# Optimization experiments

Hardware: AMD Instinct MI355X
Metric: run time of the kernel (lower is better)

Reference implementation:

```python
import jax, jax.numpy as jnp
import numpy as np
from jax import lax

N_INPUT, N_HIDDEN, N_OUTPUT = 1024, 2048, 1024
T, B = 512, 64

def setup_inputs() -> dict:
    key = jax.random.key(0)
    k_x, k_ih, k_hh, k_out = jax.random.split(key, 4)
    stdv = 1.0 / np.sqrt(N_HIDDEN)
    xs = jax.random.normal(k_x, (T, B, N_INPUT), dtype=jnp.float32)
    # torch nn.Linear weights are [out_features, in_features], init U(-stdv, stdv)
    W_ih = jax.random.uniform(k_ih, (N_HIDDEN, N_INPUT), jnp.float32, -stdv, stdv)
    W_hh = jax.random.uniform(k_hh, (N_HIDDEN, N_HIDDEN), jnp.float32, -stdv, stdv)
    W_out = jax.random.uniform(k_out, (N_OUTPUT, N_HIDDEN), jnp.float32, -stdv, stdv)
    return {"xs": xs, "W_ih": W_ih, "W_hh": W_hh, "W_out": W_out}

def reference(xs, W_ih, W_hh, W_out):
    # xs: [T, B, n_input] time-major. state starts as None -> relu(W_ih x),
    # which equals relu(W_ih x + W_hh * 0), so h0 = zeros is exact.
    n_hidden = W_hh.shape[0]
    h0 = jnp.zeros((xs.shape[1], n_hidden), dtype=xs.dtype)

    def step(h, x):
        h = jax.nn.relu(x @ W_ih.T + h @ W_hh.T)  # [B, n_hidden]
        return h, h

    _, h_seq = lax.scan(step, h0, xs)        # [T, B, n_hidden]
    ys = h_seq @ W_out.T                     # [T, B, n_output]
    return jnp.transpose(ys, (1, 0, 2))      # [B, T, n_output] (transpose(0,1))
```

## Files before the change

kernel.cpp:

```cpp
#include <hip/hip_runtime.h>
#include <hip/hip_bf16.h>
#include <stdint.h>


#define TT 512
#define BB 64
#define NIN 1024
#define NH 2048
#define NOUT 1024

typedef __attribute__((ext_vector_type(8))) short bf8;
typedef __attribute__((ext_vector_type(4))) float f4;
typedef __attribute__((ext_vector_type(4))) unsigned int u4;
typedef __attribute__((ext_vector_type(2))) unsigned long long ull2;

static __device__ __forceinline__ unsigned short f2bf(float f) {
  __hip_bfloat16 h = __float2bfloat16(f);
  return __builtin_bit_cast(unsigned short, h);
}
static __device__ __forceinline__ float bf2f(unsigned short v) {
  return __bfloat162float(__builtin_bit_cast(__hip_bfloat16, v));
}
static __device__ __forceinline__ u4 pack8(const float* f) {
  u4 r;
#pragma unroll
  for (int i = 0; i < 4; ++i) {
    unsigned lo = f2bf(f[2 * i]);
    unsigned hi = f2bf(f[2 * i + 1]);
    r[i] = lo | (hi << 16);
  }
  return r;
}

static __device__ __forceinline__ size_t sl_idx(int m, int col) {
  return (((size_t)(m >> 6) * 128 + (col >> 4)) << 10) + (size_t)(m & 63) * 16 + (col & 15);
}

template <bool ABF, bool TRANS>
__global__ void gemm_bt(const void* __restrict__ Av, const float* __restrict__ Bw,
                        void* __restrict__ Cv, int M, int N, int K) {
  constexpr int BM = 128, BN = 128, BK = 32;
  __shared__ u4 As[BM * 4];
  __shared__ u4 Bs[BN * 4];
  const int nt = N / BN;
  const int mi = (int)blockIdx.x / nt;
  const int ni = (int)blockIdx.x % nt;
  const int m0 = mi * BM, n0 = ni * BN;
  const int t = threadIdx.x;
  const int l = t & 63, w = t >> 6, wr = w >> 1, wc = w & 1;
  const int lr = l & 15, lq = l >> 4;

  f4 acc[4][4] = {};

  const int srow = t >> 1;
  const int sc0 = (t & 1) * 2;

  for (int kt = 0; kt < K; kt += BK) {
    if (ABF) {
      const unsigned short* A = (const unsigned short*)Av;
#pragma unroll
      for (int cc = 0; cc < 2; ++cc) {
        int c = sc0 + cc;
        u4 v = *(const u4*)(A + sl_idx(m0 + srow, kt + c * 8));
        As[srow * 4 + (c ^ ((srow ^ (srow >> 2)) & 3))] = v;
      }
    } else {
      const float* A = (const float*)Av;
#pragma unroll
      for (int cc = 0; cc < 2; ++cc) {
        int c = sc0 + cc;
        const float* p = A + (size_t)(m0 + srow) * K + kt + c * 8;
        float4 v0 = *(const float4*)p;
        float4 v1 = *(const float4*)(p + 4);
        float f[8] = {v0.x, v0.y, v0.z, v0.w, v1.x, v1.y, v1.z, v1.w};
        As[srow * 4 + (c ^ ((srow ^ (srow >> 2)) & 3))] = pack8(f);
      }
    }
#pragma unroll
    for (int cc = 0; cc < 2; ++cc) {
      int c = sc0 + cc;
      const float* p = Bw + (size_t)(n0 + srow) * K + kt + c * 8;
      float4 v0 = *(const float4*)p;
      float4 v1 = *(const float4*)(p + 4);
      float f[8] = {v0.x, v0.y, v0.z, v0.w, v1.x, v1.y, v1.z, v1.w};
      Bs[srow * 4 + (c ^ ((srow ^ (srow >> 2)) & 3))] = pack8(f);
    }
    __syncthreads();

    bf8 a[4], b[4];
#pragma unroll
    for (int i = 0; i < 4; ++i) {
      int ra = wr * 64 + i * 16 + lr;
      a[i] = __builtin_bit_cast(bf8, As[ra * 4 + (lq ^ ((ra ^ (ra >> 2)) & 3))]);
      int rb = wc * 64 + i * 16 + lr;
      b[i] = __builtin_bit_cast(bf8, Bs[rb * 4 + (lq ^ ((rb ^ (rb >> 2)) & 3))]);
    }
#pragma unroll
    for (int i = 0; i < 4; ++i)
#pragma unroll
      for (int j = 0; j < 4; ++j)
        acc[i][j] = __builtin_amdgcn_mfma_f32_16x16x32_bf16(a[i], b[j], acc[i][j], 0, 0, 0);
    __syncthreads();
  }

  if (TRANS) {
    float* C = (float*)Cv;
#pragma unroll
    for (int i = 0; i < 4; ++i)
#pragma unroll
      for (int j = 0; j < 4; ++j)
#pragma unroll
        for (int r = 0; r < 4; ++r) {
          int m = m0 + wr * 64 + i * 16 + lq * 4 + r;
          int n = n0 + wc * 64 + j * 16 + lr;
          C[(size_t)(m & 63) * (TT * NOUT) + (size_t)(m >> 6) * NOUT + n] = acc[i][j][r];
        }
  } else {
    unsigned short* C = (unsigned short*)Cv;
#pragma unroll
    for (int i = 0; i < 4; ++i)
#pragma unroll
      for (int j = 0; j < 4; ++j)
#pragma unroll
        for (int r = 0; r < 4; ++r) {
          int m = m0 + wr * 64 + i * 16 + lq * 4 + r;
          int n = n0 + wc * 64 + j * 16 + lr;
          C[sl_idx(m, n)] = f2bf(acc[i][j][r]);
        }
  }
}

__global__ __launch_bounds__(1024, 4) void rnn_recur(unsigned short* __restrict__ hseq,
                                                     const float* __restrict__ Whh,
                                                     unsigned* __restrict__ flags) {
  __shared__ u4 Wl[16 * 256];
  __shared__ float red[2][8][32][20];
  const int t = threadIdx.x;
  const int jb = (int)blockIdx.x & 127;
  const int bh = (int)blockIdx.x >> 7;
  const int j0 = jb * 16;

  {
    const int jl = t >> 6;
    const int c0 = (t & 63) * 4;
#pragma unroll
    for (int c = 0; c < 4; ++c) {
      int cc = c0 + c;
      const float* p = Whh + (size_t)(j0 + jl) * NH + cc * 8;
      float4 v0 = *(const float4*)p;
      float4 v1 = *(const float4*)(p + 4);
      float f[8] = {v0.x, v0.y, v0.z, v0.w, v1.x, v1.y, v1.z, v1.w};
      Wl[jl * 256 + (cc ^ (jl & 7))] = pack8(f);
    }
  }

  const int l = t & 63, w = t >> 6;
  const int lr = l & 15, lq = l >> 4;
  const int bg = w & 1, kg = w >> 1;
  const int row = bh * 32 + bg * 16 + lr;

  const int wrowL = bg * 16 + (l >> 2);
  const int wjq = l & 3;
  const size_t woff = (size_t)(bh * 32 + wrowL) * 16 + wjq * 4;

  unsigned long long pre = 0;

  __syncthreads();

  if (w < 2) {
    size_t e0 = ((size_t)jb << 10) + woff;
    unsigned long long p0 = *(const unsigned long long*)(hseq + e0);
    unsigned long long hv = 0;
#pragma unroll
    for (int i = 0; i < 4; ++i) {
      unsigned long long x = (p0 >> (16 * i)) & 0xffffull;
      if (!(x & 0x8000ull)) hv |= x << (16 * i);
    }
    __hip_atomic_store((unsigned long long*)(hseq + e0), hv, __ATOMIC_RELAXED,
                       __HIP_MEMORY_SCOPE_AGENT);
    asm volatile("s_waitcnt vmcnt(0)" ::: "memory");
    if (l == 0)
      __hip_atomic_store(flags + ((int)blockIdx.x * 2 + w), 1u, __ATOMIC_RELAXED,
                         __HIP_MEMORY_SCOPE_AGENT);
    pre = *(const unsigned long long*)(hseq + (((size_t)128 + jb) << 10) + woff);
  }

  for (int ts = 1; ts < TT; ++ts) {
    {
      const unsigned* fp = flags + ((bh * 128 + kg * 16 + lr) * 2 + bg);
      long spins = 0;
      for (;;) {
        unsigned fv = __hip_atomic_load(fp, __ATOMIC_RELAXED, __HIP_MEMORY_SCOPE_AGENT);
        if (__ballot(fv >= (unsigned)ts) == ~0ull) break;
        __builtin_amdgcn_s_sleep(1);
        if (++spins > (1L << 22)) break;
      }
    }
    asm volatile("" ::: "memory");

    const size_t tb = (size_t)(ts - 1) * 128;
    const size_t rowoff = (size_t)row * 16 + (lq & 1) * 8;
    const size_t sbase = tb + kg * 16 + (lq >> 1);
    unsigned long long ad[8];
#pragma unroll
    for (int u = 0; u < 8; ++u)
      ad[u] = (unsigned long long)(uintptr_t)(hseq + (((sbase + 2 * u) << 10) + rowoff));
    u4 av[8];
    asm volatile(
        "global_load_dwordx4 %0, %8, off sc0 sc1\n\t"
        "global_load_dwordx4 %1, %9, off sc0 sc1\n\t"
        "global_load_dwordx4 %2, %10, off sc0 sc1\n\t"
        "global_load_dwordx4 %3, %11, off sc0 sc1\n\t"
        "global_load_dwordx4 %4, %12, off sc0 sc1\n\t"
        "global_load_dwordx4 %5, %13, off sc0 sc1\n\t"
        "global_load_dwordx4 %6, %14, off sc0 sc1\n\t"
        "global_load_dwordx4 %7, %15, off sc0 sc1\n\t"
        "s_waitcnt vmcnt(0)"
        : "=&v"(av[0]), "=&v"(av[1]), "=&v"(av[2]), "=&v"(av[3]),
          "=&v"(av[4]), "=&v"(av[5]), "=&v"(av[6]), "=&v"(av[7])
        : "v"(ad[0]), "v"(ad[1]), "v"(ad[2]), "v"(ad[3]),
          "v"(ad[4]), "v"(ad[5]), "v"(ad[6]), "v"(ad[7])
        : "memory");

    f4 acc0 = {}, acc1 = {};
#pragma unroll
    for (int u = 0; u < 8; ++u) {
      bf8 af = __builtin_bit_cast(bf8, av[u]);
      int c = kg * 32 + u * 4 + lq;
      bf8 bfr = __builtin_bit_cast(bf8, Wl[lr * 256 + (c ^ (lr & 7))]);
      if (u & 1)
        acc1 = __builtin_amdgcn_mfma_f32_16x16x32_bf16(af, bfr, acc1, 0, 0, 0);
      else
        acc0 = __builtin_amdgcn_mfma_f32_16x16x32_bf16(af, bfr, acc0, 0, 0, 0);
    }
    f4 a2 = acc0 + acc1;

    const int buf = ts & 1;
#pragma unroll
    for (int r = 0; r < 4; ++r) red[buf][kg][bg * 16 + lq * 4 + r][lr] = a2[r];
    __syncthreads();

    if (w < 2) {
      f4 s = {};
#pragma unroll
      for (int q = 0; q < 8; ++q) s += *(const f4*)&red[buf][q][wrowL][wjq * 4];
      float sf[4];
#pragma unroll
      for (int i = 0; i < 4; ++i) {
        float v = s[i] + bf2f((unsigned short)((pre >> (16 * i)) & 0xffffull));
        sf[i] = v > 0.f ? v : 0.f;
      }
      unsigned lo = (unsigned)f2bf(sf[0]) | ((unsigned)f2bf(sf[1]) << 16);
      unsigned hi = (unsigned)f2bf(sf[2]) | ((unsigned)f2bf(sf[3]) << 16);
      unsigned long long hv = (unsigned long long)lo | ((unsigned long long)hi << 32);
      size_t eo = (((size_t)ts * 128 + jb) << 10) + woff;
      __hip_atomic_store((unsigned long long*)(hseq + eo), hv, __ATOMIC_RELAXED,
                         __HIP_MEMORY_SCOPE_AGENT);
      asm volatile("s_waitcnt vmcnt(0)" ::: "memory");
      if (l == 0)
        __hip_atomic_store(flags + ((int)blockIdx.x * 2 + w), (unsigned)(ts + 1),
                           __ATOMIC_RELAXED, __HIP_MEMORY_SCOPE_AGENT);
      if (ts + 1 < TT)
        pre = *(const unsigned long long*)(hseq + (((size_t)(ts + 1) * 128 + jb) << 10) + woff);
    }
  }
}

__global__ void kinit(unsigned* f) { f[threadIdx.x] = 0u; }

extern "C" void kernel_launch(void* const* d_in, const int* in_sizes, int n_in,
                              void* d_out, int out_size, void* d_ws, size_t ws_size,
                              hipStream_t stream) {
  const float* xs = (const float*)d_in[0];
  const float* Wih = (const float*)d_in[1];
  const float* Whh = (const float*)d_in[2];
  const float* Wout = (const float*)d_in[3];

  unsigned short* hseq = (unsigned short*)d_ws;
  unsigned* flags = (unsigned*)((char*)d_ws + (size_t)TT * BB * NH * 2);

  kinit<<<1, 512, 0, stream>>>(flags);

  gemm_bt<false, false><<<(TT * BB / 128) * (NH / 128), 256, 0, stream>>>(
      (const void*)xs, Wih, (void*)hseq, TT * BB, NH, NIN);

  rnn_recur<<<256, 1024, 0, stream>>>(hseq, Whh, flags);

  gemm_bt<true, true><<<(TT * BB / 128) * (NOUT / 128), 256, 0, stream>>>(
      (const void*)hseq, Wout, d_out, TT * BB, NOUT, NH);
}
```

Measured before the change: 3.930 ms.

## Fuse input projection into recurrence and use in-band sign-bit readiness flags

```diff
diff --git a/kernel.cpp b/kernel.cpp
--- a/kernel.cpp
+++ b/kernel.cpp
@@ -12,7 +12,6 @@
 typedef __attribute__((ext_vector_type(8))) short bf8;
 typedef __attribute__((ext_vector_type(4))) float f4;
 typedef __attribute__((ext_vector_type(4))) unsigned int u4;
-typedef __attribute__((ext_vector_type(2))) unsigned long long ull2;
 
 static __device__ __forceinline__ unsigned short f2bf(float f) {
   __hip_bfloat16 h = __float2bfloat16(f);
@@ -54,6 +53,7 @@
 
   const int srow = t >> 1;
   const int sc0 = (t & 1) * 2;
+  const u4 msk = {0x7fff7fffu, 0x7fff7fffu, 0x7fff7fffu, 0x7fff7fffu};
 
   for (int kt = 0; kt < K; kt += BK) {
     if (ABF) {
@@ -62,6 +62,7 @@
       for (int cc = 0; cc < 2; ++cc) {
         int c = sc0 + cc;
         u4 v = *(const u4*)(A + sl_idx(m0 + srow, kt + c * 8));
+        v &= msk;
         As[srow * 4 + (c ^ ((srow ^ (srow >> 2)) & 3))] = v;
       }
     } else {
@@ -131,9 +132,11 @@
 }
 
 __global__ __launch_bounds__(1024, 4) void rnn_recur(unsigned short* __restrict__ hseq,
+                                                     const float* __restrict__ xs,
                                                      const float* __restrict__ Whh,
-                                                     unsigned* __restrict__ flags) {
-  __shared__ u4 Wl[16 * 256];
+                                                     const float* __restrict__ Wih) {
+  __shared__ u4 Wlh[16 * 256];
+  __shared__ u4 Wli[16 * 128];
   __shared__ float red[2][8][32][20];
   const int t = threadIdx.x;
   const int jb = (int)blockIdx.x & 127;
@@ -150,7 +153,17 @@
       float4 v0 = *(const float4*)p;
       float4 v1 = *(const float4*)(p + 4);
       float f[8] = {v0.x, v0.y, v0.z, v0.w, v1.x, v1.y, v1.z, v1.w};
-      Wl[jl * 256 + (cc ^ (jl & 7))] = pack8(f);
+      Wlh[jl * 256 + (cc ^ (jl & 7))] = pack8(f);
+    }
+    const int i0 = (t & 63) * 2;
+#pragma unroll
+    for (int c = 0; c < 2; ++c) {
+      int cc = i0 + c;
+      const float* p = Wih + (size_t)(j0 + jl) * NIN + cc * 8;
+      float4 v0 = *(const float4*)p;
+      float4 v1 = *(const float4*)(p + 4);
+      float f[8] = {v0.x, v0.y, v0.z, v0.w, v1.x, v1.y, v1.z, v1.w};
+      Wli[jl * 128 + (cc ^ (jl & 7))] = pack8(f);
     }
   }
 
@@ -163,78 +176,89 @@
   const int wjq = l & 3;
   const size_t woff = (size_t)(bh * 32 + wrowL) * 16 + wjq * 4;
 
-  unsigned long long pre = 0;
+  const u4 msk = {0x7fff7fffu, 0x7fff7fffu, 0x7fff7fffu, 0x7fff7fffu};
+
+  bf8 xf[4];
+  auto load_xs = [&](int tt) {
+    const float* xp = xs + ((size_t)tt * BB + row) * NIN + kg * 128 + lq * 8;
+#pragma unroll
+    for (int u = 0; u < 4; ++u) {
+      float4 v0 = *(const float4*)(xp + u * 32);
+      float4 v1 = *(const float4*)(xp + u * 32 + 4);
+      float f[8] = {v0.x, v0.y, v0.z, v0.w, v1.x, v1.y, v1.z, v1.w};
+      xf[u] = __builtin_bit_cast(bf8, pack8(f));
+    }
+  };
+  load_xs(0);
 
   __syncthreads();
 
-  if (w < 2) {
-    size_t e0 = ((size_t)jb << 10) + woff;
-    unsigned long long p0 = *(const unsigned long long*)(hseq + e0);
-    unsigned long long hv = 0;
-#pragma unroll
-    for (int i = 0; i < 4; ++i) {
-      unsigned long long x = (p0 >> (16 * i)) & 0xffffull;
-      if (!(x & 0x8000ull)) hv |= x << (16 * i);
-    }
-    __hip_atomic_store((unsigned long long*)(hseq + e0), hv, __ATOMIC_RELAXED,
-                       __HIP_MEMORY_SCOPE_AGENT);
-    asm volatile("s_waitcnt vmcnt(0)" ::: "memory");
-    if (l == 0)
-      __hip_atomic_store(flags + ((int)blockIdx.x * 2 + w), 1u, __ATOMIC_RELAXED,
-                         __HIP_MEMORY_SCOPE_AGENT);
-    pre = *(const unsigned long long*)(hseq + (((size_t)128 + jb) << 10) + woff);
-  }
-
-  for (int ts = 1; ts < TT; ++ts) {
-    {
-      const unsigned* fp = flags + ((bh * 128 + kg * 16 + lr) * 2 + bg);
+  for (int ts = 0; ts < TT; ++ts) {
+    f4 acc0 = {}, acc1 = {};
+
+#pragma unroll
+    for (int u = 0; u < 4; ++u) {
+      int c = kg * 16 + u * 4 + lq;
+      bf8 bfr = __builtin_bit_cast(bf8, Wli[lr * 128 + (c ^ (lr & 7))]);
+      if (u & 1)
+        acc1 = __builtin_amdgcn_mfma_f32_16x16x32_bf16(xf[u], bfr, acc1, 0, 0, 0);
+      else
+        acc0 = __builtin_amdgcn_mfma_f32_16x16x32_bf16(xf[u], bfr, acc0, 0, 0, 0);
+    }
+
+    if (ts > 0) {
+      const size_t tb = (size_t)(ts - 1) * 128;
+      const size_t rowoff = (size_t)row * 16 + (lq & 1) * 8;
+      const size_t sbase = tb + kg * 16 + (lq >> 1);
+      unsigned long long ad[8];
+#pragma unroll
+      for (int u = 0; u < 8; ++u)
+        ad[u] = (unsigned long long)(uintptr_t)(hseq + (((sbase + 2 * u) << 10) + rowoff));
+      u4 av[8];
       long spins = 0;
       for (;;) {
-        unsigned fv = __hip_atomic_load(fp, __ATOMIC_RELAXED, __HIP_MEMORY_SCOPE_AGENT);
-        if (__ballot(fv >= (unsigned)ts) == ~0ull) break;
+        asm volatile(
+            "global_load_dwordx4 %0, %8, off\n\t"
+            "global_load_dwordx4 %1, %9, off\n\t"
+            "global_load_dwordx4 %2, %10, off\n\t"
+            "global_load_dwordx4 %3, %11, off\n\t"
+            "global_load_dwordx4 %4, %12, off\n\t"
+            "global_load_dwordx4 %5, %13, off\n\t"
+            "global_load_dwordx4 %6, %14, off\n\t"
+            "global_load_dwordx4 %7, %15, off\n\t"
+            "s_waitcnt vmcnt(0)"
+            : "=&v"(av[0]), "=&v"(av[1]), "=&v"(av[2]), "=&v"(av[3]),
+              "=&v"(av[4]), "=&v"(av[5]), "=&v"(av[6]), "=&v"(av[7])
+            : "v"(ad[0]), "v"(ad[1]), "v"(ad[2]), "v"(ad[3]),
+              "v"(ad[4]), "v"(ad[5]), "v"(ad[6]), "v"(ad[7])
+            : "memory");
+        unsigned m = 0xffffffffu;
+#pragma unroll
+        for (int u = 0; u < 8; ++u)
+#pragma unroll
+          for (int d = 0; d < 4; ++d) m &= av[u][d];
+        bool ok = (m & 0x80008000u) == 0x80008000u;
+        if (__ballot(ok) == ~0ull) break;
+        __builtin_amdgcn_fence(__ATOMIC_ACQUIRE, "agent");
         __builtin_amdgcn_s_sleep(1);
-        if (++spins > (1L << 22)) break;
+        if (++spins > (1L << 20)) break;
       }
-    }
-    asm volatile("" ::: "memory");
-
-    const size_t tb = (size_t)(ts - 1) * 128;
-    const size_t rowoff = (size_t)row * 16 + (lq & 1) * 8;
-    const size_t sbase = tb + kg * 16 + (lq >> 1);
-    unsigned long long ad[8];
-#pragma unroll
-    for (int u = 0; u < 8; ++u)
-      ad[u] = (unsigned long long)(uintptr_t)(hseq + (((sbase + 2 * u) << 10) + rowoff));
-    u4 av[8];
-    asm volatile(
-        "global_load_dwordx4 %0, %8, off sc0 sc1\n\t"
-        "global_load_dwordx4 %1, %9, off sc0 sc1\n\t"
-        "global_load_dwordx4 %2, %10, off sc0 sc1\n\t"
-        "global_load_dwordx4 %3, %11, off sc0 sc1\n\t"
-        "global_load_dwordx4 %4, %12, off sc0 sc1\n\t"
-        "global_load_dwordx4 %5, %13, off sc0 sc1\n\t"
-        "global_load_dwordx4 %6, %14, off sc0 sc1\n\t"
-        "global_load_dwordx4 %7, %15, off sc0 sc1\n\t"
-        "s_waitcnt vmcnt(0)"
-        : "=&v"(av[0]), "=&v"(av[1]), "=&v"(av[2]), "=&v"(av[3]),
-          "=&v"(av[4]), "=&v"(av[5]), "=&v"(av[6]), "=&v"(av[7])
-        : "v"(ad[0]), "v"(ad[1]), "v"(ad[2]), "v"(ad[3]),
-          "v"(ad[4]), "v"(ad[5]), "v"(ad[6]), "v"(ad[7])
-        : "memory");
-
-    f4 acc0 = {}, acc1 = {};
-#pragma unroll
-    for (int u = 0; u < 8; ++u) {
-      bf8 af = __builtin_bit_cast(bf8, av[u]);
-      int c = kg * 32 + u * 4 + lq;
-      bf8 bfr = __builtin_bit_cast(bf8, Wl[lr * 256 + (c ^ (lr & 7))]);
-      if (u & 1)
-        acc1 = __builtin_amdgcn_mfma_f32_16x16x32_bf16(af, bfr, acc1, 0, 0, 0);
-      else
-        acc0 = __builtin_amdgcn_mfma_f32_16x16x32_bf16(af, bfr, acc0, 0, 0, 0);
-    }
+#pragma unroll
+      for (int u = 0; u < 8; ++u) {
+        u4 v = av[u] & msk;
+        bf8 af = __builtin_bit_cast(bf8, v);
+        int c = kg * 32 + u * 4 + lq;
+        bf8 bfr = __builtin_bit_cast(bf8, Wlh[lr * 256 + (c ^ (lr & 7))]);
+        if (u & 1)
+          acc1 = __builtin_amdgcn_mfma_f32_16x16x32_bf16(af, bfr, acc1, 0, 0, 0);
+        else
+          acc0 = __builtin_amdgcn_mfma_f32_16x16x32_bf16(af, bfr, acc0, 0, 0, 0);
+      }
+    }
+
+    if (ts + 1 < TT) load_xs(ts + 1);
+
     f4 a2 = acc0 + acc1;
-
     const int buf = ts & 1;
 #pragma unroll
     for (int r = 0; r < 4; ++r) red[buf][kg][bg * 16 + lq * 4 + r][lr] = a2[r];
@@ -244,29 +268,19 @@
       f4 s = {};
 #pragma unroll
       for (int q = 0; q < 8; ++q) s += *(const f4*)&red[buf][q][wrowL][wjq * 4];
-      float sf[4];
-#pragma unroll
-      for (int i = 0; i < 4; ++i) {
-        float v = s[i] + bf2f((unsigned short)((pre >> (16 * i)) & 0xffffull));
-        sf[i] = v > 0.f ? v : 0.f;
-      }
-      unsigned lo = (unsigned)f2bf(sf[0]) | ((unsigned)f2bf(sf[1]) << 16);
-      unsigned hi = (unsigned)f2bf(sf[2]) | ((unsigned)f2bf(sf[3]) << 16);
-      unsigned long long hv = (unsigned long long)lo | ((unsigned long long)hi << 32);
+      unsigned short h0 = (s[0] > 0.f) ? f2bf(s[0]) : (unsigned short)0;
+      unsigned short h1 = (s[1] > 0.f) ? f2bf(s[1]) : (unsigned short)0;
+      unsigned short h2 = (s[2] > 0.f) ? f2bf(s[2]) : (unsigned short)0;
+      unsigned short h3 = (s[3] > 0.f) ? f2bf(s[3]) : (unsigned short)0;
+      unsigned long long hv = (unsigned long long)h0 | ((unsigned long long)h1 << 16) |
+                              ((unsigned long long)h2 << 32) | ((unsigned long long)h3 << 48);
+      hv |= 0x8000800080008000ull;
       size_t eo = (((size_t)ts * 128 + jb) << 10) + woff;
       __hip_atomic_store((unsigned long long*)(hseq + eo), hv, __ATOMIC_RELAXED,
                          __HIP_MEMORY_SCOPE_AGENT);
-      asm volatile("s_waitcnt vmcnt(0)" ::: "memory");
-      if (l == 0)
-        __hip_atomic_store(flags + ((int)blockIdx.x * 2 + w), (unsigned)(ts + 1),
-                           __ATOMIC_RELAXED, __HIP_MEMORY_SCOPE_AGENT);
-      if (ts + 1 < TT)
-        pre = *(const unsigned long long*)(hseq + (((size_t)(ts + 1) * 128 + jb) << 10) + woff);
-    }
-  }
-}
-
-__global__ void kinit(unsigned* f) { f[threadIdx.x] = 0u; }
+    }
+  }
+}
 
 extern "C" void kernel_launch(void* const* d_in, const int* in_sizes, int n_in,
                               void* d_out, int out_size, void* d_ws, size_t ws_size,
@@ -277,14 +291,10 @@
   const float* Wout = (const float*)d_in[3];
 
   unsigned short* hseq = (unsigned short*)d_ws;
-  unsigned* flags = (unsigned*)((char*)d_ws + (size_t)TT * BB * NH * 2);
-
-  kinit<<<1, 512, 0, stream>>>(flags);
-
-  gemm_bt<false, false><<<(TT * BB / 128) * (NH / 128), 256, 0, stream>>>(
-      (const void*)xs, Wih, (void*)hseq, TT * BB, NH, NIN);
-
-  rnn_recur<<<256, 1024, 0, stream>>>(hseq, Whh, flags);
+
+  hipMemsetAsync(d_ws, 0, (size_t)TT * BB * NH * 2, stream);
+
+  rnn_recur<<<256, 1024, 0, stream>>>(hseq, xs, Whh, Wih);
 
   gemm_bt<true, true><<<(TT * BB / 128) * (NOUT / 128), 256, 0, stream>>>(
       (const void*)hseq, Wout, d_out, TT * BB, NOUT, NH);
```

New measurement: 11.08 ms. 182% more time.
